# Optimization experiments

Hardware: AMD Instinct MI355X
Metric: run time of the kernel (lower is better)

Reference implementation:

```python
import jax, jax.numpy as jnp
import numpy as np

L = 16384      # sequence length
D_IN = 512     # d_input
D_H = 1024     # d_hidden
D_OUT = 512    # d_output
R_MIN = 0.0
R_MAX = 0.99
MAX_PHASE = np.pi


def setup_inputs() -> dict:
    key = jax.random.key(0)
    k_nu, k_th, k_x, k_bre, k_bim, k_cre, k_cim, k_d = jax.random.split(key, 8)
    # nu_init with parametrization='exp'
    u_nu = jax.random.uniform(k_nu, (D_H,), dtype=jnp.float32)
    nu = jnp.sqrt(u_nu * (R_MAX ** 2 - R_MIN ** 2) + R_MIN ** 2)
    u_theta = jax.random.uniform(k_th, (D_H,), dtype=jnp.float32, minval=-MAX_PHASE, maxval=MAX_PHASE)
    theta = jnp.mod(u_theta, 2 * jnp.pi)
    lamb = jnp.stack([jnp.log(-jnp.log(nu)), jnp.log(theta)], axis=0)  # [2, D_H]
    # gamma_init with parametrization='exp': nu = exp(-exp(lamb[0]))
    nu_eff = jnp.exp(-jnp.exp(lamb[0]))
    gamma = jnp.log(jnp.sqrt(1.0 - jnp.abs(nu_eff) ** 2))  # [D_H]
    # matrix_init: normal / sqrt(shape[0])
    B_re = jax.random.normal(k_bre, (D_H, D_IN), dtype=jnp.float32) / jnp.sqrt(D_H)
    B_im = jax.random.normal(k_bim, (D_H, D_IN), dtype=jnp.float32) / jnp.sqrt(D_H)
    C_re = jax.random.normal(k_cre, (D_OUT, D_H), dtype=jnp.float32) / jnp.sqrt(D_OUT)
    C_im = jax.random.normal(k_cim, (D_OUT, D_H), dtype=jnp.float32) / jnp.sqrt(D_OUT)
    D = jax.random.normal(k_d, (D_OUT, D_IN), dtype=jnp.float32) / jnp.sqrt(D_OUT)
    inputs = jax.random.normal(k_x, (L, D_IN), dtype=jnp.float32)
    return {"inputs": inputs, "lamb": lamb, "gamma": gamma,
            "B_re": B_re, "B_im": B_im, "C_re": C_re, "C_im": C_im, "D": D}


def _binary_operator_diag(q_i, q_j):
    A_i, b_i = q_i
    A_j, b_j = q_j
    return (A_j * A_i, A_j * b_i + b_j)


def reference(inputs, lamb, gamma, B_re, B_im, C_re, C_im, D):
    # parametrization='exp': lambda = exp(-exp(nu_log) + i*exp(theta_log))
    diag_lambda = jnp.exp(-jnp.exp(lamb[0]) + 1j * jnp.exp(lamb[1]))  # [D_H] complex64
    # which_gamma='learned', exp param: scale rows of B by exp(gamma)
    B_norm = jnp.exp(gamma)[:, None] * (B_re + 1j * B_im)             # [D_H, D_IN]
    # Bu_t = B_norm @ x_t for all t, as one GEMM: [L, D_H] complex
    Bu = inputs.astype(B_norm.dtype) @ B_norm.T
    Lambda_elements = jnp.broadcast_to(diag_lambda[None, :], Bu.shape)
    # diagonal linear recurrence h_t = lambda*h_{t-1} + Bu_t via parallel scan
    _, h = jax.lax.associative_scan(_binary_operator_diag, (Lambda_elements, Bu))
    C = C_re + 1j * C_im
    # y_t = Re[C h_t] + D x_t
    outputs = jnp.real(h @ C.T) + inputs @ D.T  # [L, D_OUT]
    return outputs
```

## Files before the change

### kernel.cpp

```cpp
#include <hip/hip_runtime.h>

__device__ __forceinline__ unsigned short f2b(float f) {
    unsigned int u = __builtin_bit_cast(unsigned int, f);
    unsigned int r = (u + 0x7FFFu + ((u >> 16) & 1u)) >> 16;
    return (unsigned short)r;
}
__device__ __forceinline__ float b2f(unsigned short s) {
    unsigned int u = ((unsigned int)s) << 16;
    return __builtin_bit_cast(float, u);
}

typedef __attribute__((ext_vector_type(8))) short short8;
typedef __attribute__((ext_vector_type(4))) float float4v;

#define GLD16(g, l) __builtin_amdgcn_global_load_lds(                          \
    (const __attribute__((address_space(1))) unsigned int*)(g),                \
    (__attribute__((address_space(3))) unsigned int*)(l), 16, 0, 0)

#define SEQLEN 16384
#define NCHUNK 256
#define TCHUNK 64

__global__ void xcast(const float* __restrict__ x, unsigned short* __restrict__ Hcat) {
    int id = blockIdx.x * 256 + threadIdx.x;
    int t = id >> 7;
    int k4 = (id & 127) << 2;
    float4 v = *(const float4*)(x + (long)t * 512 + k4);
    ushort4 o;
    o.x = f2b(v.x); o.y = f2b(v.y); o.z = f2b(v.z); o.w = f2b(v.w);
    *(ushort4*)(Hcat + (long)t * 2560 + 2048 + k4) = o;
}

__global__ void prep_B(const float* __restrict__ B_re, const float* __restrict__ B_im,
                       const float* __restrict__ gamma, unsigned short* __restrict__ Bcat) {
    int id = blockIdx.x * 256 + threadIdx.x;
    int n = id >> 7;
    int k4 = (id & 127) << 2;
    const float* src = (n < 1024) ? (B_re + (long)n * 512) : (B_im + (long)(n - 1024) * 512);
    float g = expf(gamma[n & 1023]);
    float4 v = *(const float4*)(src + k4);
    ushort4 o;
    o.x = f2b(v.x * g); o.y = f2b(v.y * g); o.z = f2b(v.z * g); o.w = f2b(v.w * g);
    *(ushort4*)(Bcat + (long)n * 512 + k4) = o;
}

__global__ void prep_CW(const float* __restrict__ C_re, const float* __restrict__ C_im,
                        const float* __restrict__ Dm, unsigned short* __restrict__ CW) {
    int id = blockIdx.x * 256 + threadIdx.x;
    int o = id / 640;
    int j4 = (id - o * 640) << 2;
    float4 v; float sgn = 1.0f;
    if (j4 < 1024) {
        v = *(const float4*)(C_re + (long)o * 1024 + j4);
    } else if (j4 < 2048) {
        v = *(const float4*)(C_im + (long)o * 1024 + (j4 - 1024));
        sgn = -1.0f;
    } else {
        v = *(const float4*)(Dm + (long)o * 512 + (j4 - 2048));
    }
    ushort4 w;
    w.x = f2b(v.x * sgn); w.y = f2b(v.y * sgn); w.z = f2b(v.z * sgn); w.w = f2b(v.w * sgn);
    *(ushort4*)(CW + (long)o * 2560 + j4) = w;
}

template <bool OUT_BF16>
__launch_bounds__(256)
__global__ void gemm_bt(const unsigned short* __restrict__ A, int lda,
                        const unsigned short* __restrict__ B, int ldb,
                        void* __restrict__ Cout, int ldc, int Ktot) {
    __shared__ unsigned short As[128 * 32] __attribute__((aligned(16)));
    __shared__ unsigned short Bs[128 * 32] __attribute__((aligned(16)));
    const int tid = threadIdx.x;
    const int wave = tid >> 6;
    const int lane = tid & 63;
    const long m0 = (long)blockIdx.y * 128;
    const long n0 = (long)blockIdx.x * 128;
    const int wm = (wave >> 1) * 64;
    const int wn = (wave & 1) * 64;

    const int s1 = wave * 64 + lane;
    const int r1 = s1 >> 2, c1 = (s1 & 3) * 8;
    const int s2 = s1 + 256;
    const int r2 = s2 >> 2, c2 = (s2 & 3) * 8;
    const unsigned short* Arow1 = A + (m0 + r1) * lda + c1;
    const unsigned short* Arow2 = A + (m0 + r2) * lda + c2;
    const unsigned short* Brow1 = B + (n0 + r1) * ldb + c1;
    const unsigned short* Brow2 = B + (n0 + r2) * ldb + c2;
    char* AsB1 = (char*)As + wave * 1024;
    char* AsB2 = (char*)As + 4096 + wave * 1024;
    char* BsB1 = (char*)Bs + wave * 1024;
    char* BsB2 = (char*)Bs + 4096 + wave * 1024;

    const int fr = lane & 15;
    const int fk = (lane >> 4) * 8;

    float4v acc[4][4] = {};

    for (int k0 = 0; k0 < Ktot; k0 += 32) {
        GLD16(Arow1 + k0, AsB1);
        GLD16(Arow2 + k0, AsB2);
        GLD16(Brow1 + k0, BsB1);
        GLD16(Brow2 + k0, BsB2);
        __syncthreads();
        short8 af[4], bfr[4];
#pragma unroll
        for (int i = 0; i < 4; i++) {
            af[i]  = *(const short8*)(As + (wm + i * 16 + fr) * 32 + fk);
            bfr[i] = *(const short8*)(Bs + (wn + i * 16 + fr) * 32 + fk);
        }
#pragma unroll
        for (int mi = 0; mi < 4; mi++)
#pragma unroll
            for (int ni = 0; ni < 4; ni++)
                acc[mi][ni] = __builtin_amdgcn_mfma_f32_16x16x32_bf16(af[mi], bfr[ni], acc[mi][ni], 0, 0, 0);
        __syncthreads();
    }

    const int er = (lane >> 4) * 4;
    const int ec = lane & 15;
#pragma unroll
    for (int mi = 0; mi < 4; mi++) {
#pragma unroll
        for (int r = 0; r < 4; r++) {
            long grow = m0 + wm + mi * 16 + er + r;
#pragma unroll
            for (int ni = 0; ni < 4; ni++) {
                long gcol = n0 + wn + ni * 16 + ec;
                float v = acc[mi][ni][r];
                if (OUT_BF16)
                    ((unsigned short*)Cout)[grow * ldc + gcol] = f2b(v);
                else
                    ((float*)Cout)[grow * ldc + gcol] = v;
            }
        }
    }
}

__global__ void scan_ends(const unsigned short* __restrict__ Bu,
                          const float* __restrict__ lamb,
                          float* __restrict__ E) {
    const int chunk = blockIdx.x;
    const int ch = threadIdx.x << 2;
    float lre[4], lim[4];
#pragma unroll
    for (int i = 0; i < 4; i++) {
        float nu = expf(-expf(lamb[ch + i]));
        float th = expf(lamb[1024 + ch + i]);
        lre[i] = nu * cosf(th);
        lim[i] = nu * sinf(th);
    }
    float hr[4] = {0, 0, 0, 0}, hi[4] = {0, 0, 0, 0};
    const unsigned short* base = Bu + (long)chunk * TCHUNK * 2048 + ch;
#pragma unroll 4
    for (int t = 0; t < TCHUNK; t++) {
        ushort4 br = *(const ushort4*)(base + (long)t * 2048);
        ushort4 bi = *(const ushort4*)(base + (long)t * 2048 + 1024);
        float brf[4] = {b2f(br.x), b2f(br.y), b2f(br.z), b2f(br.w)};
        float bif[4] = {b2f(bi.x), b2f(bi.y), b2f(bi.z), b2f(bi.w)};
#pragma unroll
        for (int i = 0; i < 4; i++) {
            float nr = fmaf(lre[i], hr[i], fmaf(-lim[i], hi[i], brf[i]));
            float ni = fmaf(lre[i], hi[i], fmaf(lim[i], hr[i], bif[i]));
            hr[i] = nr; hi[i] = ni;
        }
    }
    float* Ec = E + (long)chunk * 2048 + ch;
#pragma unroll
    for (int i = 0; i < 4; i++) {
        Ec[i] = hr[i];
        Ec[1024 + i] = hi[i];
    }
}

__global__ void carry(const float* __restrict__ lamb, const float* __restrict__ E,
                      float* __restrict__ Kc) {
    const int ch = blockIdx.x * 256 + threadIdx.x;
    double nu = exp(-exp((double)lamb[ch]));
    double th = exp((double)lamb[1024 + ch]);
    double lr = nu * cos(th), li = nu * sin(th);
#pragma unroll
    for (int i = 0; i < 6; i++) {
        double rr = lr * lr - li * li;
        double ii = 2.0 * lr * li;
        lr = rr; li = ii;
    }
    float tre = (float)lr, tim = (float)li;
    float hr = 0.0f, hi = 0.0f;
#pragma unroll 8
    for (int c = 0; c < NCHUNK; c++) {
        Kc[(long)c * 2048 + ch] = hr;
        Kc[(long)c * 2048 + 1024 + ch] = hi;
        float er = E[(long)c * 2048 + ch];
        float ei = E[(long)c * 2048 + 1024 + ch];
        float nr = fmaf(tre, hr, fmaf(-tim, hi, er));
        float ni = fmaf(tre, hi, fmaf(tim, hr, ei));
        hr = nr; hi = ni;
    }
}

__global__ void scan_apply(const unsigned short* __restrict__ Bu,
                           const float* __restrict__ lamb,
                           const float* __restrict__ Kc,
                           unsigned short* __restrict__ Hcat) {
    const int chunk = blockIdx.x;
    const int ch = threadIdx.x << 2;
    float lre[4], lim[4];
#pragma unroll
    for (int i = 0; i < 4; i++) {
        float nu = expf(-expf(lamb[ch + i]));
        float th = expf(lamb[1024 + ch + i]);
        lre[i] = nu * cosf(th);
        lim[i] = nu * sinf(th);
    }
    float hr[4], hi[4];
#pragma unroll
    for (int i = 0; i < 4; i++) {
        hr[i] = Kc[(long)chunk * 2048 + ch + i];
        hi[i] = Kc[(long)chunk * 2048 + 1024 + ch + i];
    }
    const unsigned short* base = Bu + (long)chunk * TCHUNK * 2048 + ch;
    unsigned short* Hc = Hcat + (long)chunk * TCHUNK * 2560 + ch;
#pragma unroll 4
    for (int t = 0; t < TCHUNK; t++) {
        ushort4 br = *(const ushort4*)(base + (long)t * 2048);
        ushort4 bi = *(const ushort4*)(base + (long)t * 2048 + 1024);
        float brf[4] = {b2f(br.x), b2f(br.y), b2f(br.z), b2f(br.w)};
        float bif[4] = {b2f(bi.x), b2f(bi.y), b2f(bi.z), b2f(bi.w)};
#pragma unroll
        for (int i = 0; i < 4; i++) {
            float nr = fmaf(lre[i], hr[i], fmaf(-lim[i], hi[i], brf[i]));
            float ni = fmaf(lre[i], hi[i], fmaf(lim[i], hr[i], bif[i]));
            hr[i] = nr; hi[i] = ni;
        }
        ushort4 orv, oiv;
        orv.x = f2b(hr[0]); orv.y = f2b(hr[1]); orv.z = f2b(hr[2]); orv.w = f2b(hr[3]);
        oiv.x = f2b(hi[0]); oiv.y = f2b(hi[1]); oiv.z = f2b(hi[2]); oiv.w = f2b(hi[3]);
        *(ushort4*)(Hc + (long)t * 2560) = orv;
        *(ushort4*)(Hc + (long)t * 2560 + 1024) = oiv;
    }
}

extern "C" void kernel_launch(void* const* d_in, const int* in_sizes, int n_in,
                              void* d_out, int out_size, void* d_ws, size_t ws_size,
                              hipStream_t stream) {
    const float* x     = (const float*)d_in[0];
    const float* lamb  = (const float*)d_in[1];
    const float* gamma = (const float*)d_in[2];
    const float* B_re  = (const float*)d_in[3];
    const float* B_im  = (const float*)d_in[4];
    const float* C_re  = (const float*)d_in[5];
    const float* C_im  = (const float*)d_in[6];
    const float* Dm    = (const float*)d_in[7];

    char* ws = (char*)d_ws;
    unsigned short* Bu   = (unsigned short*)ws;
    unsigned short* Hcat = (unsigned short*)(ws + 67108864);
    float* E  = (float*)(ws + 67108864 + 83886080);
    float* Kc = E + (long)NCHUNK * 2048;
    unsigned short* Bcat = (unsigned short*)((char*)Kc + 2097152);
    unsigned short* CW   = Bcat + (long)2048 * 512;

    xcast<<<8192, 256, 0, stream>>>(x, Hcat);
    prep_B<<<1024, 256, 0, stream>>>(B_re, B_im, gamma, Bcat);
    prep_CW<<<1280, 256, 0, stream>>>(C_re, C_im, Dm, CW);
    gemm_bt<true><<<dim3(16, 128), 256, 0, stream>>>(Hcat + 2048, 2560, Bcat, 512, Bu, 2048, 512);
    scan_ends<<<NCHUNK, 256, 0, stream>>>(Bu, lamb, E);
    carry<<<4, 256, 0, stream>>>(lamb, E, Kc);
    scan_apply<<<NCHUNK, 256, 0, stream>>>(Bu, lamb, Kc, Hcat);
    gemm_bt<false><<<dim3(4, 128), 256, 0, stream>>>(Hcat, 2560, CW, 2560, d_out, 512, 2560);
}
```

Before: 285.9 us.

## Fuse prep kernels, scan in place in Hcat, remap GEMM blocks per XCD, halve chunk size

Merges the three prep kernels into one launch, writes the first GEMM's Bu output directly into the Hcat buffer and runs the scan in place, which drops the separate Bu buffer and a copy. Both GEMMs now use a 1D grid with a block-to-tile mapping that gives each XCD a contiguous band of rows, aiming for better L2 reuse. The scan chunk count doubles to 512 with 32 steps each, and the carry power loop is adjusted to lambda^32 to match, giving more parallelism in the scan kernels at the cost of a longer serial carry loop.

```diff
diff --git a/kernel.cpp b/kernel.cpp
--- a/kernel.cpp
+++ b/kernel.cpp
@@ -18,63 +18,76 @@
     (__attribute__((address_space(3))) unsigned int*)(l), 16, 0, 0)
 
 #define SEQLEN 16384
-#define NCHUNK 256
-#define TCHUNK 64
-
-__global__ void xcast(const float* __restrict__ x, unsigned short* __restrict__ Hcat) {
-    int id = blockIdx.x * 256 + threadIdx.x;
-    int t = id >> 7;
-    int k4 = (id & 127) << 2;
-    float4 v = *(const float4*)(x + (long)t * 512 + k4);
-    ushort4 o;
-    o.x = f2b(v.x); o.y = f2b(v.y); o.z = f2b(v.z); o.w = f2b(v.w);
-    *(ushort4*)(Hcat + (long)t * 2560 + 2048 + k4) = o;
-}
-
-__global__ void prep_B(const float* __restrict__ B_re, const float* __restrict__ B_im,
-                       const float* __restrict__ gamma, unsigned short* __restrict__ Bcat) {
-    int id = blockIdx.x * 256 + threadIdx.x;
-    int n = id >> 7;
-    int k4 = (id & 127) << 2;
-    const float* src = (n < 1024) ? (B_re + (long)n * 512) : (B_im + (long)(n - 1024) * 512);
-    float g = expf(gamma[n & 1023]);
-    float4 v = *(const float4*)(src + k4);
-    ushort4 o;
-    o.x = f2b(v.x * g); o.y = f2b(v.y * g); o.z = f2b(v.z * g); o.w = f2b(v.w * g);
-    *(ushort4*)(Bcat + (long)n * 512 + k4) = o;
-}
-
-__global__ void prep_CW(const float* __restrict__ C_re, const float* __restrict__ C_im,
-                        const float* __restrict__ Dm, unsigned short* __restrict__ CW) {
-    int id = blockIdx.x * 256 + threadIdx.x;
-    int o = id / 640;
-    int j4 = (id - o * 640) << 2;
-    float4 v; float sgn = 1.0f;
-    if (j4 < 1024) {
-        v = *(const float4*)(C_re + (long)o * 1024 + j4);
-    } else if (j4 < 2048) {
-        v = *(const float4*)(C_im + (long)o * 1024 + (j4 - 1024));
-        sgn = -1.0f;
+#define NCHUNK 512
+#define TCHUNK 32
+#define LDH 2560
+
+__global__ void prep_all(const float* __restrict__ x,
+                         const float* __restrict__ B_re, const float* __restrict__ B_im,
+                         const float* __restrict__ gamma,
+                         const float* __restrict__ C_re, const float* __restrict__ C_im,
+                         const float* __restrict__ Dm,
+                         unsigned short* __restrict__ Hcat,
+                         unsigned short* __restrict__ Bcat,
+                         unsigned short* __restrict__ CW) {
+    int b = blockIdx.x;
+    if (b < 8192) {
+        int id = b * 256 + threadIdx.x;
+        int t = id >> 7;
+        int k4 = (id & 127) << 2;
+        float4 v = *(const float4*)(x + (long)t * 512 + k4);
+        ushort4 o;
+        o.x = f2b(v.x); o.y = f2b(v.y); o.z = f2b(v.z); o.w = f2b(v.w);
+        *(ushort4*)(Hcat + (long)t * LDH + 2048 + k4) = o;
+    } else if (b < 9216) {
+        int id = (b - 8192) * 256 + threadIdx.x;
+        int n = id >> 7;
+        int k4 = (id & 127) << 2;
+        const float* src = (n < 1024) ? (B_re + (long)n * 512) : (B_im + (long)(n - 1024) * 512);
+        float g = expf(gamma[n & 1023]);
+        float4 v = *(const float4*)(src + k4);
+        ushort4 o;
+        o.x = f2b(v.x * g); o.y = f2b(v.y * g); o.z = f2b(v.z * g); o.w = f2b(v.w * g);
+        *(ushort4*)(Bcat + (long)n * 512 + k4) = o;
     } else {
-        v = *(const float4*)(Dm + (long)o * 512 + (j4 - 2048));
-    }
-    ushort4 w;
-    w.x = f2b(v.x * sgn); w.y = f2b(v.y * sgn); w.z = f2b(v.z * sgn); w.w = f2b(v.w * sgn);
-    *(ushort4*)(CW + (long)o * 2560 + j4) = w;
+        int id = (b - 9216) * 256 + threadIdx.x;
+        int o = id / 640;
+        int j4 = (id - o * 640) << 2;
+        float4 v; float sgn = 1.0f;
+        if (j4 < 1024) {
+            v = *(const float4*)(C_re + (long)o * 1024 + j4);
+        } else if (j4 < 2048) {
+            v = *(const float4*)(C_im + (long)o * 1024 + (j4 - 1024));
+            sgn = -1.0f;
+        } else {
+            v = *(const float4*)(Dm + (long)o * 512 + (j4 - 2048));
+        }
+        ushort4 w;
+        w.x = f2b(v.x * sgn); w.y = f2b(v.y * sgn); w.z = f2b(v.z * sgn); w.w = f2b(v.w * sgn);
+        *(ushort4*)(CW + (long)o * 2560 + j4) = w;
+    }
 }
 
 template <bool OUT_BF16>
 __launch_bounds__(256)
 __global__ void gemm_bt(const unsigned short* __restrict__ A, int lda,
                         const unsigned short* __restrict__ B, int ldb,
-                        void* __restrict__ Cout, int ldc, int Ktot) {
+                        void* __restrict__ Cout, int ldc, int Ktot,
+                        int nbx_shift, int nby_d8) {
     __shared__ unsigned short As[128 * 32] __attribute__((aligned(16)));
     __shared__ unsigned short Bs[128 * 32] __attribute__((aligned(16)));
     const int tid = threadIdx.x;
     const int wave = tid >> 6;
     const int lane = tid & 63;
-    const long m0 = (long)blockIdx.y * 128;
-    const long n0 = (long)blockIdx.x * 128;
+
+    const int bid = blockIdx.x;
+    const int xcd = bid & 7;
+    const int g = bid >> 3;
+    const int bx = g & ((1 << nbx_shift) - 1);
+    const int by = xcd * nby_d8 + (g >> nbx_shift);
+    const long m0 = (long)by * 128;
+    const long n0 = (long)bx * 128;
+
     const int wm = (wave >> 1) * 64;
     const int wn = (wave & 1) * 64;
 
@@ -136,7 +149,7 @@
     }
 }
 
-__global__ void scan_ends(const unsigned short* __restrict__ Bu,
+__global__ void scan_ends(const unsigned short* __restrict__ Hcat,
                           const float* __restrict__ lamb,
                           float* __restrict__ E) {
     const int chunk = blockIdx.x;
@@ -150,11 +163,11 @@
         lim[i] = nu * sinf(th);
     }
     float hr[4] = {0, 0, 0, 0}, hi[4] = {0, 0, 0, 0};
-    const unsigned short* base = Bu + (long)chunk * TCHUNK * 2048 + ch;
+    const unsigned short* base = Hcat + (long)chunk * TCHUNK * LDH + ch;
 #pragma unroll 4
     for (int t = 0; t < TCHUNK; t++) {
-        ushort4 br = *(const ushort4*)(base + (long)t * 2048);
-        ushort4 bi = *(const ushort4*)(base + (long)t * 2048 + 1024);
+        ushort4 br = *(const ushort4*)(base + (long)t * LDH);
+        ushort4 bi = *(const ushort4*)(base + (long)t * LDH + 1024);
         float brf[4] = {b2f(br.x), b2f(br.y), b2f(br.z), b2f(br.w)};
         float bif[4] = {b2f(bi.x), b2f(bi.y), b2f(bi.z), b2f(bi.w)};
 #pragma unroll
@@ -179,7 +192,7 @@
     double th = exp((double)lamb[1024 + ch]);
     double lr = nu * cos(th), li = nu * sin(th);
 #pragma unroll
-    for (int i = 0; i < 6; i++) {
+    for (int i = 0; i < 5; i++) {
         double rr = lr * lr - li * li;
         double ii = 2.0 * lr * li;
         lr = rr; li = ii;
@@ -198,10 +211,9 @@
     }
 }
 
-__global__ void scan_apply(const unsigned short* __restrict__ Bu,
+__global__ void scan_apply(unsigned short* __restrict__ Hcat,
                            const float* __restrict__ lamb,
-                           const float* __restrict__ Kc,
-                           unsigned short* __restrict__ Hcat) {
+                           const float* __restrict__ Kc) {
     const int chunk = blockIdx.x;
     const int ch = threadIdx.x << 2;
     float lre[4], lim[4];
@@ -218,12 +230,11 @@
         hr[i] = Kc[(long)chunk * 2048 + ch + i];
         hi[i] = Kc[(long)chunk * 2048 + 1024 + ch + i];
     }
-    const unsigned short* base = Bu + (long)chunk * TCHUNK * 2048 + ch;
-    unsigned short* Hc = Hcat + (long)chunk * TCHUNK * 2560 + ch;
+    unsigned short* base = Hcat + (long)chunk * TCHUNK * LDH + ch;
 #pragma unroll 4
     for (int t = 0; t < TCHUNK; t++) {
-        ushort4 br = *(const ushort4*)(base + (long)t * 2048);
-        ushort4 bi = *(const ushort4*)(base + (long)t * 2048 + 1024);
+        ushort4 br = *(const ushort4*)(base + (long)t * LDH);
+        ushort4 bi = *(const ushort4*)(base + (long)t * LDH + 1024);
         float brf[4] = {b2f(br.x), b2f(br.y), b2f(br.z), b2f(br.w)};
         float bif[4] = {b2f(bi.x), b2f(bi.y), b2f(bi.z), b2f(bi.w)};
 #pragma unroll
@@ -235,8 +246,8 @@
         ushort4 orv, oiv;
         orv.x = f2b(hr[0]); orv.y = f2b(hr[1]); orv.z = f2b(hr[2]); orv.w = f2b(hr[3]);
         oiv.x = f2b(hi[0]); oiv.y = f2b(hi[1]); oiv.z = f2b(hi[2]); oiv.w = f2b(hi[3]);
-        *(ushort4*)(Hc + (long)t * 2560) = orv;
-        *(ushort4*)(Hc + (long)t * 2560 + 1024) = oiv;
+        *(ushort4*)(base + (long)t * LDH) = orv;
+        *(ushort4*)(base + (long)t * LDH + 1024) = oiv;
     }
 }
 
@@ -253,19 +264,18 @@
     const float* Dm    = (const float*)d_in[7];
 
     char* ws = (char*)d_ws;
-    unsigned short* Bu   = (unsigned short*)ws;
-    unsigned short* Hcat = (unsigned short*)(ws + 67108864);
-    float* E  = (float*)(ws + 67108864 + 83886080);
+    unsigned short* Hcat = (unsigned short*)ws;
+    float* E  = (float*)(ws + 83886080);
     float* Kc = E + (long)NCHUNK * 2048;
-    unsigned short* Bcat = (unsigned short*)((char*)Kc + 2097152);
+    unsigned short* Bcat = (unsigned short*)((char*)Kc + 4194304);
     unsigned short* CW   = Bcat + (long)2048 * 512;
 
-    xcast<<<8192, 256, 0, stream>>>(x, Hcat);
-    prep_B<<<1024, 256, 0, stream>>>(B_re, B_im, gamma, Bcat);
-    prep_CW<<<1280, 256, 0, stream>>>(C_re, C_im, Dm, CW);
-    gemm_bt<true><<<dim3(16, 128), 256, 0, stream>>>(Hcat + 2048, 2560, Bcat, 512, Bu, 2048, 512);
-    scan_ends<<<NCHUNK, 256, 0, stream>>>(Bu, lamb, E);
+    prep_all<<<10496, 256, 0, stream>>>(x, B_re, B_im, gamma, C_re, C_im, Dm, Hcat, Bcat, CW);
+    gemm_bt<true><<<2048, 256, 0, stream>>>(Hcat + 2048, LDH, Bcat, 512, Hcat, LDH, 512,
+                                            4, 16);
+    scan_ends<<<NCHUNK, 256, 0, stream>>>(Hcat, lamb, E);
     carry<<<4, 256, 0, stream>>>(lamb, E, Kc);
-    scan_apply<<<NCHUNK, 256, 0, stream>>>(Bu, lamb, Kc, Hcat);
-    gemm_bt<false><<<dim3(4, 128), 256, 0, stream>>>(Hcat, 2560, CW, 2560, d_out, 512, 2560);
-}
+    scan_apply<<<NCHUNK, 256, 0, stream>>>(Hcat, lamb, Kc);
+    gemm_bt<false><<<512, 256, 0, stream>>>(Hcat, LDH, CW, 2560, d_out, 512, 2560,
+                                            2, 16);
+}
```

Result: no change. 290.3 us (+1.5%).
